# Performance work log

Measured on AMD Instinct MI355X. Metric: run time of the kernel, lower is better.

The kernel has to match this reference:

```python
import jax, jax.numpy as jnp
import numpy as np

B, T, IN, H = 128, 128, 64, 512  # batch, seq_len, input_size, encoded_size==hidden_size


def _cell(x, h, c, Wih, Whh, bih, bhh):
    # PyTorch LSTM gate order: i, f, g, o
    g = x @ Wih.T + h @ Whh.T + bih + bhh
    i, f, gg, o = jnp.split(g, 4, axis=-1)
    c = jax.nn.sigmoid(f) * c + jax.nn.sigmoid(i) * jnp.tanh(gg)
    h = jax.nn.sigmoid(o) * jnp.tanh(c)
    return h, c


def _lstm_layer(xs, Wih, Whh, bih, bhh):
    # xs: [T, B, din] -> ys: [T, B, H], zero initial state (as in the torch module)
    b = xs.shape[1]
    hdim = Whh.shape[1]
    h0 = jnp.zeros((b, hdim), xs.dtype)
    c0 = jnp.zeros((b, hdim), xs.dtype)

    def step(carry, x):
        h, c = _cell(x, carry[0], carry[1], Wih, Whh, bih, bhh)
        return (h, c), h

    _, ys = jax.lax.scan(step, (h0, c0), xs)
    return ys


def setup_inputs() -> dict:
    key = jax.random.key(0)
    ks = jax.random.split(key, 18)
    s = 1.0 / np.sqrt(H)  # torch LSTM default init scale
    r = lambda k, shp: jax.random.uniform(k, shp, jnp.float32, -s, s)
    return {
        "x": jax.random.normal(ks[0], (B, T, IN), jnp.float32),
        # encoder layer 0 (input IN) and layer 1 (input H)
        "eW_ih0": r(ks[1], (4 * H, IN)), "eW_hh0": r(ks[2], (4 * H, H)),
        "eb_ih0": r(ks[3], (4 * H,)), "eb_hh0": r(ks[4], (4 * H,)),
        "eW_ih1": r(ks[5], (4 * H, H)), "eW_hh1": r(ks[6], (4 * H, H)),
        "eb_ih1": r(ks[7], (4 * H,)), "eb_hh1": r(ks[8], (4 * H,)),
        # decoder layer 0 (input H = encoded_size) and layer 1
        "dW_ih0": r(ks[9], (4 * H, H)), "dW_hh0": r(ks[10], (4 * H, H)),
        "db_ih0": r(ks[11], (4 * H,)), "db_hh0": r(ks[12], (4 * H,)),
        "dW_ih1": r(ks[13], (4 * H, H)), "dW_hh1": r(ks[14], (4 * H, H)),
        "db_ih1": r(ks[15], (4 * H,)), "db_hh1": r(ks[16], (4 * H,)),
        # output projection
        "fc_W": r(ks[17], (IN, H)), "fc_b": jnp.zeros((IN,), jnp.float32),
    }


def reference(x, eW_ih0, eW_hh0, eb_ih0, eb_hh0, eW_ih1, eW_hh1, eb_ih1, eb_hh1,
              dW_ih0, dW_hh0, db_ih0, db_hh0, dW_ih1, dW_hh1, db_ih1, db_hh1,
              fc_W, fc_b):
    b, t = x.shape[0], x.shape[1]
    xs = jnp.swapaxes(x, 0, 1)  # [T, B, IN]
    # 2-layer encoder, take last timestep of top layer
    y0 = _lstm_layer(xs, eW_ih0, eW_hh0, eb_ih0, eb_hh0)
    y1 = _lstm_layer(y0, eW_ih1, eW_hh1, eb_ih1, eb_hh1)
    z = y1[-1]  # [B, H] constant decoder input each step
    hdim = dW_hh0.shape[1]
    zero = jnp.zeros((b, hdim), x.dtype)

    def step(carry, _):
        h0, c0, h1, c1 = carry
        h0, c0 = _cell(z, h0, c0, dW_ih0, dW_hh0, db_ih0, db_hh0)
        h1, c1 = _cell(h0, h1, c1, dW_ih1, dW_hh1, db_ih1, db_hh1)
        return (h0, c0, h1, c1), h1

    _, hs = jax.lax.scan(step, (zero, zero, zero, zero), None, length=t)  # [T, B, H]
    out = jnp.einsum('tbh,ih->tbi', hs, fc_W) + fc_b
    return jnp.swapaxes(out, 0, 1)  # [B, T, IN]
```

## Files before the change

kernel.cpp:

```cpp
#include <hip/hip_runtime.h>
#include <cstdint>

#define TT 128

typedef _Float16 f16;
typedef _Float16 f16x8 __attribute__((ext_vector_type(8)));
typedef float f32x4 __attribute__((ext_vector_type(4)));
typedef unsigned int u32;
typedef unsigned long long u64;

#define PIN(v) asm volatile("" : "+v"(v))

#define OFF_H0    16384
#define OFF_H1    (OFF_H0 + 262144)
#define OFF_D0    (OFF_H1 + 262144)
#define OFF_D1    (OFF_D0 + 262144)
#define OFF_XH    (OFF_D1 + 262144)
#define OFF_HS    (OFF_XH + 2097152)

#define L_SA   0
#define L_SB   24576
#define L_TOT  65536

#define MFMA16(a,b,c) __builtin_amdgcn_mfma_f32_16x16x32_f16((a),(b),(c),0,0,0)

__device__ __forceinline__ float sigm(float x){ return 1.f/(1.f+__expf(-x)); }
__device__ __forceinline__ float tanhft(float x){ return 1.f - 2.f/(__expf(2.f*x)+1.f); }

__device__ __forceinline__ f16x8 wfrag(const float* __restrict__ src, int K, int srow,
                                       int k, int j){
  const float* p = src + srow*K + (k<<5) + (j<<3);
  float4 v0 = *(const float4*)p;
  float4 v1 = *(const float4*)(p+4);
  f16x8 r;
  r[0]=(f16)v0.x; r[1]=(f16)v0.y; r[2]=(f16)v0.z; r[3]=(f16)v0.w;
  r[4]=(f16)v1.x; r[5]=(f16)v1.y; r[6]=(f16)v1.z; r[7]=(f16)v1.w;
  return r;
}

__device__ __forceinline__ void stage1(const char* R, char* S, int tid){
  const int cgs = tid >> 3, rr = (tid & 7) << 1;
  const char* gp = R + cgs*512 + rr*32;
  char* sp = S + cgs*768 + rr*48;
  u64 t0[8];
#pragma unroll
  for (int e = 0; e < 2; ++e)
#pragma unroll
    for (int i = 0; i < 4; ++i)
      t0[e*4+i] = __hip_atomic_load((const u64*)(gp + e*32 + i*8),
                                    __ATOMIC_RELAXED, __HIP_MEMORY_SCOPE_AGENT);
#pragma unroll
  for (int e = 0; e < 2; ++e)
#pragma unroll
    for (int i = 0; i < 4; ++i)
      *(u64*)(sp + e*48 + i*8) = t0[e*4+i];
}

__device__ __forceinline__ void stage2(const char* R0, const char* R1,
                                       char* SA, char* SB, int tid){
  const int cgs = tid >> 3, rr = (tid & 7) << 1;
  const char* g0 = R0 + cgs*512 + rr*32;
  const char* g1 = R1 + cgs*512 + rr*32;
  char* s0 = SA + cgs*768 + rr*48;
  char* s1 = SB + cgs*768 + rr*48;
  u64 t0[8], t1[8];
#pragma unroll
  for (int e = 0; e < 2; ++e)
#pragma unroll
    for (int i = 0; i < 4; ++i)
      t0[e*4+i] = __hip_atomic_load((const u64*)(g0 + e*32 + i*8),
                                    __ATOMIC_RELAXED, __HIP_MEMORY_SCOPE_AGENT);
#pragma unroll
  for (int e = 0; e < 2; ++e)
#pragma unroll
    for (int i = 0; i < 4; ++i)
      t1[e*4+i] = __hip_atomic_load((const u64*)(g1 + e*32 + i*8),
                                    __ATOMIC_RELAXED, __HIP_MEMORY_SCOPE_AGENT);
#pragma unroll
  for (int e = 0; e < 2; ++e)
#pragma unroll
    for (int i = 0; i < 4; ++i)
      *(u64*)(s0 + e*48 + i*8) = t0[e*4+i];
#pragma unroll
  for (int e = 0; e < 2; ++e)
#pragma unroll
    for (int i = 0; i < 4; ++i)
      *(u64*)(s1 + e*48 + i*8) = t1[e*4+i];
}

__device__ __forceinline__ void gbar(u32* cnt, int tid, u32 target32){
  __syncthreads();
  if (tid == 0){
    u32 c = __hip_atomic_fetch_add(cnt, 1, __ATOMIC_RELAXED, __HIP_MEMORY_SCOPE_AGENT) + 1;
    while (c < target32){
      __builtin_amdgcn_s_sleep(1);
      c = __hip_atomic_load(cnt, __ATOMIC_RELAXED, __HIP_MEMORY_SCOPE_AGENT);
    }
  }
  __syncthreads();
}

__global__ void cvt_x(const float* __restrict__ x, char* __restrict__ ws){
  int i = blockIdx.x*256 + threadIdx.x;
  int p = i & 3, b = (i >> 2) & 127, t = i >> 9;
  const float* s = x + (((b<<7) + t)<<6) + (p<<4);
  float4 v0 = *(const float4*)s,     v1 = *(const float4*)(s+4);
  float4 v2 = *(const float4*)(s+8), v3 = *(const float4*)(s+12);
  f16x8 h0, h1;
  h0[0]=(f16)v0.x; h0[1]=(f16)v0.y; h0[2]=(f16)v0.z; h0[3]=(f16)v0.w;
  h0[4]=(f16)v1.x; h0[5]=(f16)v1.y; h0[6]=(f16)v1.z; h0[7]=(f16)v1.w;
  h1[0]=(f16)v2.x; h1[1]=(f16)v2.y; h1[2]=(f16)v2.z; h1[3]=(f16)v2.w;
  h1[4]=(f16)v3.x; h1[5]=(f16)v3.y; h1[6]=(f16)v3.z; h1[7]=(f16)v3.w;
  char* d = ws + OFF_XH + ((((t<<3) + (b>>4))<<4) + (b&15))*128 + (p<<5);
  *(f16x8*)d = h0;
  *(f16x8*)(d+16) = h1;
}

__global__ __launch_bounds__(256, 1) void lstm_persist(
    const float* __restrict__ eWih0, const float* __restrict__ eWhh0,
    const float* __restrict__ ebi0,  const float* __restrict__ ebh0,
    const float* __restrict__ eWih1, const float* __restrict__ eWhh1,
    const float* __restrict__ ebi1,  const float* __restrict__ ebh1,
    const float* __restrict__ dWih0, const float* __restrict__ dWhh0,
    const float* __restrict__ dbi0,  const float* __restrict__ dbh0,
    const float* __restrict__ dWih1, const float* __restrict__ dWhh1,
    const float* __restrict__ dbi1,  const float* __restrict__ dbh1,
    const float* __restrict__ fcW,   const float* __restrict__ fcb,
    float* __restrict__ out, char* __restrict__ ws)
{
  __shared__ __align__(16) char lds[L_TOT];
  const int tid  = threadIdx.x;
  const int wg   = blockIdx.x;
  const int g    = wg & 7;
  const int cg   = wg >> 3;
  const int b0   = g << 4;
  const int lane = tid & 63, w = tid >> 6;
  const int j    = lane >> 4;
  const int arow = lane & 15;
  const int bq   = lane & 15;
  const int srow = ((bq&3)<<9) + (cg<<4) + (w<<2) + (bq>>2);
  const int lq   = lane & 3;
  const int hcc  = (lane >> 2) & 3;
  const int row_c = ((lane>>4)<<2) + lq;

  u32* cnt = (u32*)(ws + (g<<6));
  char* H0 = ws + OFF_H0;  char* H1 = ws + OFF_H1;
  char* D0 = ws + OFF_D0;  char* D1 = ws + OFF_D1;
  const char* XH = ws + OFF_XH;
  char* HS = ws + OFF_HS;
  char* SA = lds + 0; char* SB = lds + L_SB;

  const int abase = ((j>>1)*768) + arow*48 + ((j&1)<<4);
  const int hst = cg*512 + row_c*32 + (w<<3);

  f16x8 wA[16], wB[16], wC[16], wX0, wX1;
#pragma unroll
  for (int k = 0; k < 16; ++k){
    wA[k] = wfrag(eWhh0, 512, srow, k, j);  PIN(wA[k]);
    wB[k] = wfrag(eWih1, 512, srow, k, j);  PIN(wB[k]);
    wC[k] = wfrag(eWhh1, 512, srow, k, j);  PIN(wC[k]);
  }
  wX0 = wfrag(eWih0, 64, srow, 0, j);  PIN(wX0);
  wX1 = wfrag(eWih0, 64, srow, 1, j);  PIN(wX1);
  float B0r[4], B1r[4];
#pragma unroll
  for (int e = 0; e < 4; ++e){
    int bi = (e<<9) + (cg<<4) + (w<<2) + hcc;
    B0r[e] = ebi0[bi] + ebh0[bi];  PIN(B0r[e]);
    B1r[e] = ebi1[bi] + ebh1[bi];  PIN(B1r[e]);
  }

  auto qtr = [&](f32x4 a) -> f32x4 {
    float s0 = __shfl_xor(a[1],1), s1 = __shfl_xor(a[0],1);
    float s2 = __shfl_xor(a[3],1), s3 = __shfl_xor(a[2],1);
    bool o1 = lane & 1;
    float c0 = o1 ? s0 : a[0];
    float c1 = o1 ? a[1] : s1;
    float c2 = o1 ? s2 : a[2];
    float c3 = o1 ? a[3] : s3;
    float u0 = __shfl_xor(c2,2), u1 = __shfl_xor(c3,2);
    float u2 = __shfl_xor(c0,2), u3 = __shfl_xor(c1,2);
    bool o2 = lane & 2;
    f32x4 t;
    t[0] = o2 ? u0 : c0;
    t[1] = o2 ? u1 : c1;
    t[2] = o2 ? c2 : u2;
    t[3] = o2 ? c3 : u3;
    return t;
  };

  float c0v = 0.f, c1v = 0.f;
  u32 bt = 0;

  for (int s = 0; s <= TT; ++s){
    const bool d0 = (s < TT), d1 = (s >= 1);
    const char* R0 = H0 + (((s&1)<<3) + g)*16384;
    const char* R1 = H1 + (((s&1)<<3) + g)*16384;
    char* W0 = H0 + ((((s+1)&1)<<3) + g)*16384;
    char* W1 = H1 + ((((s+1)&1)<<3) + g)*16384;

    stage2(R0, R1, SA, SB, tid);
    f16x8 xa0, xa1;
    if (d0){
      const char* xg = XH + (((s<<3) + g)<<11) + arow*128 + (j<<4);
      xa0 = *(const f16x8*)(xg);
      xa1 = *(const f16x8*)(xg + 64);
    }
    __syncthreads();

    f32x4 acc0 = {0.f,0.f,0.f,0.f}, acc1 = {0.f,0.f,0.f,0.f};
    if (d0){
      acc0 = MFMA16(xa0, wX0, acc0);
      acc0 = MFMA16(xa1, wX1, acc0);
    }
#pragma unroll
    for (int k = 0; k < 16; ++k){
      f16x8 a0 = *(const f16x8*)(SA + k*1536 + abase);
      f16x8 a1 = *(const f16x8*)(SB + k*1536 + abase);
      acc0 = MFMA16(a0, wA[k], acc0);
      acc1 = MFMA16(a0, wB[k], acc1);
      acc1 = MFMA16(a1, wC[k], acc1);
    }

    if (d0){
      f32x4 t = qtr(acc0);
      float gi = sigm(t[0]+B0r[0]), gf = sigm(t[1]+B0r[1]);
      float gg = tanhft(t[2]+B0r[2]), go = sigm(t[3]+B0r[3]);
      c0v = gf*c0v + gi*gg;
      float h = go * tanhft(c0v);
      union { f16 hf; unsigned short su; } cv; cv.hf = (f16)h;
      u32 v = cv.su;
      u32 p = v | (((u32)(unsigned short)__shfl_xor((int)v, 4)) << 16);
      u32 q = (u32)__shfl_xor((int)p, 8);
      if (!(lane & 12)){
        u64 pk = (u64)p | ((u64)q << 32);
        __hip_atomic_store((u64*)(W0 + hst), pk,
                           __ATOMIC_RELAXED, __HIP_MEMORY_SCOPE_AGENT);
      }
    }
    if (d1){
      f32x4 t = qtr(acc1);
      float gi = sigm(t[0]+B1r[0]), gf = sigm(t[1]+B1r[1]);
      float gg = tanhft(t[2]+B1r[2]), go = sigm(t[3]+B1r[3]);
      c1v = gf*c1v + gi*gg;
      float h = go * tanhft(c1v);
      union { f16 hf; unsigned short su; } cv; cv.hf = (f16)h;
      u32 v = cv.su;
      u32 p = v | (((u32)(unsigned short)__shfl_xor((int)v, 4)) << 16);
      u32 q = (u32)__shfl_xor((int)p, 8);
      if (!(lane & 12)){
        u64 pk = (u64)p | ((u64)q << 32);
        __hip_atomic_store((u64*)(W1 + hst), pk,
                           __ATOMIC_RELAXED, __HIP_MEMORY_SCOPE_AGENT);
      }
    }
    gbar(cnt, tid, (++bt) << 5);
  }

  f32x4 zx;
  {
    stage1(H1 + (8 + g)*16384, SA, tid);
    f16x8 wZ[16];
#pragma unroll
    for (int k = 0; k < 16; ++k) wZ[k] = wfrag(dWih0, 512, srow, k, j);
    float zb = dbi0[srow] + dbh0[srow];
    zx[0]=zb; zx[1]=zb; zx[2]=zb; zx[3]=zb;
    __syncthreads();
#pragma unroll
    for (int k = 0; k < 16; ++k)
      zx = MFMA16(*(const f16x8*)(SA + k*1536 + abase), wZ[k], zx);
  }

#pragma unroll
  for (int k = 0; k < 16; ++k){
    wA[k] = wfrag(dWhh0, 512, srow, k, j);  PIN(wA[k]);
    wB[k] = wfrag(dWih1, 512, srow, k, j);  PIN(wB[k]);
    wC[k] = wfrag(dWhh1, 512, srow, k, j);  PIN(wC[k]);
  }
#pragma unroll
  for (int e = 0; e < 4; ++e){
    int bi = (e<<9) + (cg<<4) + (w<<2) + hcc;
    B1r[e] = dbi1[bi] + dbh1[bi];  PIN(B1r[e]);
  }
  c0v = 0.f; c1v = 0.f;

  for (int s = 0; s <= TT; ++s){
    const bool d0 = (s < TT), d1 = (s >= 1);
    const char* R0 = D0 + (((s&1)<<3) + g)*16384;
    const char* R1 = D1 + (((s&1)<<3) + g)*16384;
    char* W0 = D0 + ((((s+1)&1)<<3) + g)*16384;
    char* W1 = D1 + ((((s+1)&1)<<3) + g)*16384;

    stage2(R0, R1, SA, SB, tid);
    __syncthreads();

    f32x4 acc0 = zx, acc1 = {0.f,0.f,0.f,0.f};
#pragma unroll
    for (int k = 0; k < 16; ++k){
      f16x8 a0 = *(const f16x8*)(SA + k*1536 + abase);
      f16x8 a1 = *(const f16x8*)(SB + k*1536 + abase);
      acc0 = MFMA16(a0, wA[k], acc0);
      acc1 = MFMA16(a0, wB[k], acc1);
      acc1 = MFMA16(a1, wC[k], acc1);
    }

    if (d0){
      f32x4 t = qtr(acc0);
      float gi = sigm(t[0]), gf = sigm(t[1]);
      float gg = tanhft(t[2]), go = sigm(t[3]);
      c0v = gf*c0v + gi*gg;
      float h = go * tanhft(c0v);
      union { f16 hf; unsigned short su; } cv; cv.hf = (f16)h;
      u32 v = cv.su;
      u32 p = v | (((u32)(unsigned short)__shfl_xor((int)v, 4)) << 16);
      u32 q = (u32)__shfl_xor((int)p, 8);
      if (!(lane & 12)){
        u64 pk = (u64)p | ((u64)q << 32);
        __hip_atomic_store((u64*)(W0 + hst), pk,
                           __ATOMIC_RELAXED, __HIP_MEMORY_SCOPE_AGENT);
      }
    }
    if (d1){
      f32x4 t = qtr(acc1);
      float gi = sigm(t[0]+B1r[0]), gf = sigm(t[1]+B1r[1]);
      float gg = tanhft(t[2]+B1r[2]), go = sigm(t[3]+B1r[3]);
      c1v = gf*c1v + gi*gg;
      float h = go * tanhft(c1v);
      union { f16 hf; unsigned short su; } cv; cv.hf = (f16)h;
      u32 v = cv.su;
      u32 p = v | (((u32)(unsigned short)__shfl_xor((int)v, 4)) << 16);
      u32 q = (u32)__shfl_xor((int)p, 8);
      if (!(lane & 12)){
        u64 pk = (u64)p | ((u64)q << 32);
        __hip_atomic_store((u64*)(W1 + hst), pk,
                           __ATOMIC_RELAXED, __HIP_MEMORY_SCOPE_AGENT);
        __hip_atomic_store((u64*)(HS + (((s-1)<<7) + b0 + row_c)*1024 + cg*32 + (w<<3)), pk,
                           __ATOMIC_RELAXED, __HIP_MEMORY_SCOPE_AGENT);
      }
    }
    gbar(cnt, tid, (++bt) << 5);
  }

  __builtin_amdgcn_fence(__ATOMIC_ACQUIRE, "agent");
  __syncthreads();

  for (int qd = tid; qd < 8192; qd += 256){
    int i = qd >> 7, kq = qd & 127;
    float4 v = *(const float4*)(fcW + (i<<9) + (kq<<2));
    f16* p = (f16*)(lds + (i<<10) + (kq<<3));
    p[0]=(f16)v.x; p[1]=(f16)v.y; p[2]=(f16)v.z; p[3]=(f16)v.w;
  }
  __syncthreads();
  {
    int t  = (cg<<2) + w;
    int r  = (lane >> 2) & 15;
    int iq = lane & 3;
    const char* hsrow = HS + (((t<<7) + b0 + r)<<10);
    float acc[16];
#pragma unroll
    for (int ii = 0; ii < 16; ++ii) acc[ii] = 0.f;
    for (int k8 = 0; k8 < 64; ++k8){
      f16x8 hv = *(const f16x8*)(hsrow + (k8<<4));
#pragma unroll
      for (int ii = 0; ii < 16; ++ii){
        f16x8 wv = *(const f16x8*)(lds + (((iq<<4)+ii)<<10) + (k8<<4));
#pragma unroll
        for (int jj = 0; jj < 8; ++jj) acc[ii] += (float)hv[jj] * (float)wv[jj];
      }
    }
#pragma unroll
    for (int ii = 0; ii < 16; ++ii){
      int i = (iq<<4) + ii;
      out[((((b0+r)<<7) + t)<<6) + i] = acc[ii] + fcb[i];
    }
  }
}

extern "C" void kernel_launch(void* const* d_in, const int* in_sizes, int n_in,
                              void* d_out, int out_size, void* d_ws, size_t ws_size,
                              hipStream_t stream){
  const float* x     = (const float*)d_in[0];
  const float* eWih0 = (const float*)d_in[1];
  const float* eWhh0 = (const float*)d_in[2];
  const float* ebi0  = (const float*)d_in[3];
  const float* ebh0  = (const float*)d_in[4];
  const float* eWih1 = (const float*)d_in[5];
  const float* eWhh1 = (const float*)d_in[6];
  const float* ebi1  = (const float*)d_in[7];
  const float* ebh1  = (const float*)d_in[8];
  const float* dWih0 = (const float*)d_in[9];
  const float* dWhh0 = (const float*)d_in[10];
  const float* dbi0  = (const float*)d_in[11];
  const float* dbh0  = (const float*)d_in[12];
  const float* dWih1 = (const float*)d_in[13];
  const float* dWhh1 = (const float*)d_in[14];
  const float* dbi1  = (const float*)d_in[15];
  const float* dbh1  = (const float*)d_in[16];
  const float* fcW   = (const float*)d_in[17];
  const float* fcb   = (const float*)d_in[18];
  char* ws = (char*)d_ws;

  hipMemsetAsync(d_ws, 0, OFF_XH, stream);
  cvt_x<<<256, 256, 0, stream>>>(x, ws);
  lstm_persist<<<256, 256, 0, stream>>>(eWih0,eWhh0,ebi0,ebh0,eWih1,eWhh1,ebi1,ebh1,
                                        dWih0,dWhh0,dbi0,dbh0,dWih1,dWhh1,dbi1,dbh1,
                                        fcW,fcb,(float*)d_out,ws);
}
```

Measured before the change: 1.386 ms.

## Split batch into sixteen groups of eight and run two workgroups per CU

Changes the persistent LSTM kernel from 8 batch groups of 16 rows to 16 groups of 8 rows, doubling the grid to 512 workgroups with launch bounds allowing two per CU. Halves the staged hidden-state tiles, LDS strides, x-conversion layout and output projection work per workgroup, and removes the register pin asm. The aim is shorter per-step staging and more concurrent groups. In exchange, each 16x16 MFMA now has only 8 valid rows, so half its work is wasted. Two workgroups per CU must also share the matrix units, and the ~192 VGPRs of resident weights risk spilling under the tighter register budget.

```diff
diff --git a/kernel.cpp b/kernel.cpp
--- a/kernel.cpp
+++ b/kernel.cpp
@@ -8,8 +8,6 @@
 typedef float f32x4 __attribute__((ext_vector_type(4)));
 typedef unsigned int u32;
 typedef unsigned long long u64;
-
-#define PIN(v) asm volatile("" : "+v"(v))
 
 #define OFF_H0    16384
 #define OFF_H1    (OFF_H0 + 262144)
@@ -18,8 +16,7 @@
 #define OFF_XH    (OFF_D1 + 262144)
 #define OFF_HS    (OFF_XH + 2097152)
 
-#define L_SA   0
-#define L_SB   24576
+#define L_SB   12288
 #define L_TOT  65536
 
 #define MFMA16(a,b,c) __builtin_amdgcn_mfma_f32_16x16x32_f16((a),(b),(c),0,0,0)
@@ -39,53 +36,39 @@
 }
 
 __device__ __forceinline__ void stage1(const char* R, char* S, int tid){
-  const int cgs = tid >> 3, rr = (tid & 7) << 1;
-  const char* gp = R + cgs*512 + rr*32;
-  char* sp = S + cgs*768 + rr*48;
-  u64 t0[8];
-#pragma unroll
-  for (int e = 0; e < 2; ++e)
-#pragma unroll
-    for (int i = 0; i < 4; ++i)
-      t0[e*4+i] = __hip_atomic_load((const u64*)(gp + e*32 + i*8),
-                                    __ATOMIC_RELAXED, __HIP_MEMORY_SCOPE_AGENT);
-#pragma unroll
-  for (int e = 0; e < 2; ++e)
-#pragma unroll
-    for (int i = 0; i < 4; ++i)
-      *(u64*)(sp + e*48 + i*8) = t0[e*4+i];
+  const int cgs = tid >> 3, row = tid & 7;
+  const char* gp = R + cgs*256 + row*32;
+  char* sp = S + cgs*384 + row*48;
+  u64 t0[4];
+#pragma unroll
+  for (int i = 0; i < 4; ++i)
+    t0[i] = __hip_atomic_load((const u64*)(gp + i*8),
+                              __ATOMIC_RELAXED, __HIP_MEMORY_SCOPE_AGENT);
+#pragma unroll
+  for (int i = 0; i < 4; ++i)
+    *(u64*)(sp + i*8) = t0[i];
 }
 
 __device__ __forceinline__ void stage2(const char* R0, const char* R1,
                                        char* SA, char* SB, int tid){
-  const int cgs = tid >> 3, rr = (tid & 7) << 1;
-  const char* g0 = R0 + cgs*512 + rr*32;
-  const char* g1 = R1 + cgs*512 + rr*32;
-  char* s0 = SA + cgs*768 + rr*48;
-  char* s1 = SB + cgs*768 + rr*48;
-  u64 t0[8], t1[8];
-#pragma unroll
-  for (int e = 0; e < 2; ++e)
-#pragma unroll
-    for (int i = 0; i < 4; ++i)
-      t0[e*4+i] = __hip_atomic_load((const u64*)(g0 + e*32 + i*8),
-                                    __ATOMIC_RELAXED, __HIP_MEMORY_SCOPE_AGENT);
-#pragma unroll
-  for (int e = 0; e < 2; ++e)
-#pragma unroll
-    for (int i = 0; i < 4; ++i)
-      t1[e*4+i] = __hip_atomic_load((const u64*)(g1 + e*32 + i*8),
-                                    __ATOMIC_RELAXED, __HIP_MEMORY_SCOPE_AGENT);
-#pragma unroll
-  for (int e = 0; e < 2; ++e)
-#pragma unroll
-    for (int i = 0; i < 4; ++i)
-      *(u64*)(s0 + e*48 + i*8) = t0[e*4+i];
-#pragma unroll
-  for (int e = 0; e < 2; ++e)
-#pragma unroll
-    for (int i = 0; i < 4; ++i)
-      *(u64*)(s1 + e*48 + i*8) = t1[e*4+i];
+  const int cgs = tid >> 3, row = tid & 7;
+  const char* g0 = R0 + cgs*256 + row*32;
+  const char* g1 = R1 + cgs*256 + row*32;
+  char* s0 = SA + cgs*384 + row*48;
+  char* s1 = SB + cgs*384 + row*48;
+  u64 t0[4], t1[4];
+#pragma unroll
+  for (int i = 0; i < 4; ++i)
+    t0[i] = __hip_atomic_load((const u64*)(g0 + i*8),
+                              __ATOMIC_RELAXED, __HIP_MEMORY_SCOPE_AGENT);
+#pragma unroll
+  for (int i = 0; i < 4; ++i)
+    t1[i] = __hip_atomic_load((const u64*)(g1 + i*8),
+                              __ATOMIC_RELAXED, __HIP_MEMORY_SCOPE_AGENT);
+#pragma unroll
+  for (int i = 0; i < 4; ++i) *(u64*)(s0 + i*8) = t0[i];
+#pragma unroll
+  for (int i = 0; i < 4; ++i) *(u64*)(s1 + i*8) = t1[i];
 }
 
 __device__ __forceinline__ void gbar(u32* cnt, int tid, u32 target32){
@@ -101,22 +84,17 @@
 }
 
 __global__ void cvt_x(const float* __restrict__ x, char* __restrict__ ws){
-  int i = blockIdx.x*256 + threadIdx.x;
-  int p = i & 3, b = (i >> 2) & 127, t = i >> 9;
-  const float* s = x + (((b<<7) + t)<<6) + (p<<4);
-  float4 v0 = *(const float4*)s,     v1 = *(const float4*)(s+4);
-  float4 v2 = *(const float4*)(s+8), v3 = *(const float4*)(s+12);
-  f16x8 h0, h1;
-  h0[0]=(f16)v0.x; h0[1]=(f16)v0.y; h0[2]=(f16)v0.z; h0[3]=(f16)v0.w;
-  h0[4]=(f16)v1.x; h0[5]=(f16)v1.y; h0[6]=(f16)v1.z; h0[7]=(f16)v1.w;
-  h1[0]=(f16)v2.x; h1[1]=(f16)v2.y; h1[2]=(f16)v2.z; h1[3]=(f16)v2.w;
-  h1[4]=(f16)v3.x; h1[5]=(f16)v3.y; h1[6]=(f16)v3.z; h1[7]=(f16)v3.w;
-  char* d = ws + OFF_XH + ((((t<<3) + (b>>4))<<4) + (b&15))*128 + (p<<5);
-  *(f16x8*)d = h0;
-  *(f16x8*)(d+16) = h1;
-}
-
-__global__ __launch_bounds__(256, 1) void lstm_persist(
+  int idx = blockIdx.x*256 + threadIdx.x;
+  int chunk = idx & 7, b = (idx >> 3) & 127, t = idx >> 10;
+  const float* s = x + (((b<<7) + t)<<6) + (chunk<<3);
+  float4 v0 = *(const float4*)s, v1 = *(const float4*)(s+4);
+  f16x8 h;
+  h[0]=(f16)v0.x; h[1]=(f16)v0.y; h[2]=(f16)v0.z; h[3]=(f16)v0.w;
+  h[4]=(f16)v1.x; h[5]=(f16)v1.y; h[6]=(f16)v1.z; h[7]=(f16)v1.w;
+  *(f16x8*)(ws + OFF_XH + ((t<<4) + (b>>3))*1024 + (b&7)*128 + (chunk<<4)) = h;
+}
+
+__global__ __launch_bounds__(256, 2) void lstm_persist(
     const float* __restrict__ eWih0, const float* __restrict__ eWhh0,
     const float* __restrict__ ebi0,  const float* __restrict__ ebh0,
     const float* __restrict__ eWih1, const float* __restrict__ eWhh1,
@@ -131,17 +109,18 @@
   __shared__ __align__(16) char lds[L_TOT];
   const int tid  = threadIdx.x;
   const int wg   = blockIdx.x;
-  const int g    = wg & 7;
-  const int cg   = wg >> 3;
-  const int b0   = g << 4;
+  const int g    = wg >> 5;
+  const int cg   = wg & 31;
+  const int b0   = g << 3;
   const int lane = tid & 63, w = tid >> 6;
   const int j    = lane >> 4;
-  const int arow = lane & 15;
+  const int arow = (lane & 15) & 7;
   const int bq   = lane & 15;
   const int srow = ((bq&3)<<9) + (cg<<4) + (w<<2) + (bq>>2);
   const int lq   = lane & 3;
   const int hcc  = (lane >> 2) & 3;
   const int row_c = ((lane>>4)<<2) + lq;
+  const bool vrow = (lane < 32);
 
   u32* cnt = (u32*)(ws + (g<<6));
   char* H0 = ws + OFF_H0;  char* H1 = ws + OFF_H1;
@@ -150,24 +129,24 @@
   char* HS = ws + OFF_HS;
   char* SA = lds + 0; char* SB = lds + L_SB;
 
-  const int abase = ((j>>1)*768) + arow*48 + ((j&1)<<4);
-  const int hst = cg*512 + row_c*32 + (w<<3);
+  const int abase = ((j>>1)*384) + arow*48 + ((j&1)<<4);
+  const int hst = cg*256 + row_c*32 + (w<<3);
 
   f16x8 wA[16], wB[16], wC[16], wX0, wX1;
 #pragma unroll
   for (int k = 0; k < 16; ++k){
-    wA[k] = wfrag(eWhh0, 512, srow, k, j);  PIN(wA[k]);
-    wB[k] = wfrag(eWih1, 512, srow, k, j);  PIN(wB[k]);
-    wC[k] = wfrag(eWhh1, 512, srow, k, j);  PIN(wC[k]);
-  }
-  wX0 = wfrag(eWih0, 64, srow, 0, j);  PIN(wX0);
-  wX1 = wfrag(eWih0, 64, srow, 1, j);  PIN(wX1);
+    wA[k] = wfrag(eWhh0, 512, srow, k, j);
+    wB[k] = wfrag(eWih1, 512, srow, k, j);
+    wC[k] = wfrag(eWhh1, 512, srow, k, j);
+  }
+  wX0 = wfrag(eWih0, 64, srow, 0, j);
+  wX1 = wfrag(eWih0, 64, srow, 1, j);
   float B0r[4], B1r[4];
 #pragma unroll
   for (int e = 0; e < 4; ++e){
     int bi = (e<<9) + (cg<<4) + (w<<2) + hcc;
-    B0r[e] = ebi0[bi] + ebh0[bi];  PIN(B0r[e]);
-    B1r[e] = ebi1[bi] + ebh1[bi];  PIN(B1r[e]);
+    B0r[e] = ebi0[bi] + ebh0[bi];
+    B1r[e] = ebi1[bi] + ebh1[bi];
   }
 
   auto qtr = [&](f32x4 a) -> f32x4 {
@@ -194,15 +173,15 @@
 
   for (int s = 0; s <= TT; ++s){
     const bool d0 = (s < TT), d1 = (s >= 1);
-    const char* R0 = H0 + (((s&1)<<3) + g)*16384;
-    const char* R1 = H1 + (((s&1)<<3) + g)*16384;
-    char* W0 = H0 + ((((s+1)&1)<<3) + g)*16384;
-    char* W1 = H1 + ((((s+1)&1)<<3) + g)*16384;
+    const char* R0 = H0 + (((s&1)<<4) + g)*8192;
+    const char* R1 = H1 + (((s&1)<<4) + g)*8192;
+    char* W0 = H0 + ((((s+1)&1)<<4) + g)*8192;
+    char* W1 = H1 + ((((s+1)&1)<<4) + g)*8192;
 
     stage2(R0, R1, SA, SB, tid);
     f16x8 xa0, xa1;
     if (d0){
-      const char* xg = XH + (((s<<3) + g)<<11) + arow*128 + (j<<4);
+      const char* xg = XH + ((s<<4) + g)*1024 + arow*128 + (j<<4);
       xa0 = *(const f16x8*)(xg);
       xa1 = *(const f16x8*)(xg + 64);
     }
@@ -215,8 +194,8 @@
     }
 #pragma unroll
     for (int k = 0; k < 16; ++k){
-      f16x8 a0 = *(const f16x8*)(SA + k*1536 + abase);
-      f16x8 a1 = *(const f16x8*)(SB + k*1536 + abase);
+      f16x8 a0 = *(const f16x8*)(SA + k*768 + abase);
+      f16x8 a1 = *(const f16x8*)(SB + k*768 + abase);
       acc0 = MFMA16(a0, wA[k], acc0);
       acc1 = MFMA16(a0, wB[k], acc1);
       acc1 = MFMA16(a1, wC[k], acc1);
@@ -232,7 +211,7 @@
       u32 v = cv.su;
       u32 p = v | (((u32)(unsigned short)__shfl_xor((int)v, 4)) << 16);
       u32 q = (u32)__shfl_xor((int)p, 8);
-      if (!(lane & 12)){
+      if (!(lane & 12) && vrow){
         u64 pk = (u64)p | ((u64)q << 32);
         __hip_atomic_store((u64*)(W0 + hst), pk,
                            __ATOMIC_RELAXED, __HIP_MEMORY_SCOPE_AGENT);
@@ -248,7 +227,7 @@
       u32 v = cv.su;
       u32 p = v | (((u32)(unsigned short)__shfl_xor((int)v, 4)) << 16);
       u32 q = (u32)__shfl_xor((int)p, 8);
-      if (!(lane & 12)){
+      if (!(lane & 12) && vrow){
         u64 pk = (u64)p | ((u64)q << 32);
         __hip_atomic_store((u64*)(W1 + hst), pk,
                            __ATOMIC_RELAXED, __HIP_MEMORY_SCOPE_AGENT);
@@ -259,7 +238,7 @@
 
   f32x4 zx;
   {
-    stage1(H1 + (8 + g)*16384, SA, tid);
+    stage1(H1 + (16 + g)*8192, SA, tid);
     f16x8 wZ[16];
 #pragma unroll
     for (int k = 0; k < 16; ++k) wZ[k] = wfrag(dWih0, 512, srow, k, j);
@@ -268,28 +247,28 @@
     __syncthreads();
 #pragma unroll
     for (int k = 0; k < 16; ++k)
-      zx = MFMA16(*(const f16x8*)(SA + k*1536 + abase), wZ[k], zx);
+      zx = MFMA16(*(const f16x8*)(SA + k*768 + abase), wZ[k], zx);
   }
 
 #pragma unroll
   for (int k = 0; k < 16; ++k){
-    wA[k] = wfrag(dWhh0, 512, srow, k, j);  PIN(wA[k]);
-    wB[k] = wfrag(dWih1, 512, srow, k, j);  PIN(wB[k]);
-    wC[k] = wfrag(dWhh1, 512, srow, k, j);  PIN(wC[k]);
+    wA[k] = wfrag(dWhh0, 512, srow, k, j);
+    wB[k] = wfrag(dWih1, 512, srow, k, j);
+    wC[k] = wfrag(dWhh1, 512, srow, k, j);
   }
 #pragma unroll
   for (int e = 0; e < 4; ++e){
     int bi = (e<<9) + (cg<<4) + (w<<2) + hcc;
-    B1r[e] = dbi1[bi] + dbh1[bi];  PIN(B1r[e]);
+    B1r[e] = dbi1[bi] + dbh1[bi];
   }
   c0v = 0.f; c1v = 0.f;
 
   for (int s = 0; s <= TT; ++s){
     const bool d0 = (s < TT), d1 = (s >= 1);
-    const char* R0 = D0 + (((s&1)<<3) + g)*16384;
-    const char* R1 = D1 + (((s&1)<<3) + g)*16384;
-    char* W0 = D0 + ((((s+1)&1)<<3) + g)*16384;
-    char* W1 = D1 + ((((s+1)&1)<<3) + g)*16384;
+    const char* R0 = D0 + (((s&1)<<4) + g)*8192;
+    const char* R1 = D1 + (((s&1)<<4) + g)*8192;
+    char* W0 = D0 + ((((s+1)&1)<<4) + g)*8192;
+    char* W1 = D1 + ((((s+1)&1)<<4) + g)*8192;
 
     stage2(R0, R1, SA, SB, tid);
     __syncthreads();
@@ -297,8 +276,8 @@
     f32x4 acc0 = zx, acc1 = {0.f,0.f,0.f,0.f};
 #pragma unroll
     for (int k = 0; k < 16; ++k){
-      f16x8 a0 = *(const f16x8*)(SA + k*1536 + abase);
-      f16x8 a1 = *(const f16x8*)(SB + k*1536 + abase);
+      f16x8 a0 = *(const f16x8*)(SA + k*768 + abase);
+      f16x8 a1 = *(const f16x8*)(SB + k*768 + abase);
       acc0 = MFMA16(a0, wA[k], acc0);
       acc1 = MFMA16(a0, wB[k], acc1);
       acc1 = MFMA16(a1, wC[k], acc1);
@@ -314,7 +293,7 @@
       u32 v = cv.su;
       u32 p = v | (((u32)(unsigned short)__shfl_xor((int)v, 4)) << 16);
       u32 q = (u32)__shfl_xor((int)p, 8);
-      if (!(lane & 12)){
+      if (!(lane & 12) && vrow){
         u64 pk = (u64)p | ((u64)q << 32);
         __hip_atomic_store((u64*)(W0 + hst), pk,
                            __ATOMIC_RELAXED, __HIP_MEMORY_SCOPE_AGENT);
@@ -330,7 +309,7 @@
       u32 v = cv.su;
       u32 p = v | (((u32)(unsigned short)__shfl_xor((int)v, 4)) << 16);
       u32 q = (u32)__shfl_xor((int)p, 8);
-      if (!(lane & 12)){
+      if (!(lane & 12) && vrow){
         u64 pk = (u64)p | ((u64)q << 32);
         __hip_atomic_store((u64*)(W1 + hst), pk,
                            __ATOMIC_RELAXED, __HIP_MEMORY_SCOPE_AGENT);
@@ -353,24 +332,24 @@
   __syncthreads();
   {
     int t  = (cg<<2) + w;
-    int r  = (lane >> 2) & 15;
-    int iq = lane & 3;
+    int r  = lane >> 3;
+    int iq = lane & 7;
     const char* hsrow = HS + (((t<<7) + b0 + r)<<10);
-    float acc[16];
-#pragma unroll
-    for (int ii = 0; ii < 16; ++ii) acc[ii] = 0.f;
+    float acc[8];
+#pragma unroll
+    for (int ii = 0; ii < 8; ++ii) acc[ii] = 0.f;
     for (int k8 = 0; k8 < 64; ++k8){
       f16x8 hv = *(const f16x8*)(hsrow + (k8<<4));
 #pragma unroll
-      for (int ii = 0; ii < 16; ++ii){
-        f16x8 wv = *(const f16x8*)(lds + (((iq<<4)+ii)<<10) + (k8<<4));
+      for (int ii = 0; ii < 8; ++ii){
+        f16x8 wv = *(const f16x8*)(lds + (((iq<<3)+ii)<<10) + (k8<<4));
 #pragma unroll
         for (int jj = 0; jj < 8; ++jj) acc[ii] += (float)hv[jj] * (float)wv[jj];
       }
     }
 #pragma unroll
-    for (int ii = 0; ii < 16; ++ii){
-      int i = (iq<<4) + ii;
+    for (int ii = 0; ii < 8; ++ii){
+      int i = (iq<<3) + ii;
       out[((((b0+r)<<7) + t)<<6) + i] = acc[ii] + fcb[i];
     }
   }
@@ -401,8 +380,8 @@
   char* ws = (char*)d_ws;
 
   hipMemsetAsync(d_ws, 0, OFF_XH, stream);
-  cvt_x<<<256, 256, 0, stream>>>(x, ws);
-  lstm_persist<<<256, 256, 0, stream>>>(eWih0,eWhh0,ebi0,ebh0,eWih1,eWhh1,ebi1,ebh1,
+  cvt_x<<<512, 256, 0, stream>>>(x, ws);
+  lstm_persist<<<512, 256, 0, stream>>>(eWih0,eWhh0,ebi0,ebh0,eWih1,eWhh1,ebi1,ebh1,
                                         dWih0,dWhh0,dbi0,dbh0,dWih1,dWhh1,dbi1,dbh1,
                                         fcW,fcb,(float*)d_out,ws);
 }
```

Result: slower. 1.928 ms (+39.1%).
